# Kernel tuning notes

Hardware: AMD Instinct MI355X
Metric: run time of the kernel (lower is better)

Reference implementation:

```python
import jax, jax.numpy as jnp
import numpy as np

H = 1024  # lstm_hidden_dim
E = 1024  # embedding_size
T = 512   # seq_len
B = 128   # batch


def setup_inputs() -> dict:
    key = jax.random.key(0)
    k0, k1, k2, k3 = jax.random.split(key, 4)
    bound = 1.0 / np.sqrt(H)
    embeds = jax.random.normal(k0, (T, B, E), dtype=jnp.float32)
    # Stacked gate weights in order [g, i, f, o]; same math as 8 separate GEMMs.
    W_x = jax.random.uniform(k1, (E, 4 * H), jnp.float32, -bound, bound)
    W_h = jax.random.uniform(k2, (H, 4 * H), jnp.float32, -bound, bound)
    b = jax.random.uniform(k3, (4 * H,), jnp.float32, -bound, bound)
    b = b.at[2 * H:3 * H].add(1.0)  # forget-gate bias +1
    return {"embeds": embeds, "W_x": W_x, "W_h": W_h, "b": b}


def reference(embeds, W_x, W_h, b):
    Tn, Bn, _ = embeds.shape
    # Batch all input projections into one big GEMM (same math as per-step GEMMs).
    xproj = jnp.einsum('tbe,ef->tbf', embeds, W_x) + b  # [T, B, 4H]
    h0 = jnp.zeros((Bn, H), embeds.dtype)
    c0 = jnp.zeros((Bn, H), embeds.dtype)

    def step(carry, xp):
        h, c = carry
        z = xp + h @ W_h  # [B, 4H]
        g = jnp.tanh(z[:, :H])
        i = jax.nn.sigmoid(z[:, H:2 * H])
        f = jax.nn.sigmoid(z[:, 2 * H:3 * H])
        o = jax.nn.sigmoid(z[:, 3 * H:])
        c_new = g * i + c * f
        h_new = jnp.tanh(c_new) * o
        # Original module records h BEFORE the update at step t (h_prev).
        return (h_new, c_new), h

    _, h_total = jax.lax.scan(step, (h0, c0), xproj)
    return h_total  # [T, B, H], h_total[0] is zeros
```

## Files before the change

kernel.cpp:

```cpp
#include <hip/hip_runtime.h>
#include <hip/hip_bf16.h>

typedef __attribute__((ext_vector_type(8)))  short          bf16x8;
typedef __attribute__((ext_vector_type(4)))  float          f32x4;
typedef __attribute__((ext_vector_type(8)))  unsigned short us8;

__device__ __forceinline__ unsigned short f2b(float f) {
  union { __hip_bfloat16 h; unsigned short u; } v;
  v.h = __float2bfloat16(f);
  return v.u;
}
__device__ __forceinline__ float b2f(unsigned short u) {
  union { unsigned u; float f; } v; v.u = ((unsigned)u) << 16; return v.f;
}
__device__ __forceinline__ float sigf(float x) {
  return __builtin_amdgcn_rcpf(1.f + __expf(-x));
}
__device__ __forceinline__ float tanhf_(float x) {
  return 2.f * __builtin_amdgcn_rcpf(1.f + __expf(-2.f * x)) - 1.f;
}


__global__ __launch_bounds__(256) void conv_e(const float* __restrict__ in,
                                              unsigned short* __restrict__ out) {
  const size_t i = ((size_t)blockIdx.x * 256 + threadIdx.x) * 8;
  const float4 v0 = *(const float4*)(in + i);
  const float4 v1 = *(const float4*)(in + i + 4);
  us8 o;
  o[0]=f2b(v0.x); o[1]=f2b(v0.y); o[2]=f2b(v0.z); o[3]=f2b(v0.w);
  o[4]=f2b(v1.x); o[5]=f2b(v1.y); o[6]=f2b(v1.z); o[7]=f2b(v1.w);
  *(us8*)(out + i) = o;
}

__global__ __launch_bounds__(256) void conv_wT(const float* __restrict__ W,
                                               unsigned short* __restrict__ WT) {
  __shared__ float tile[64][65];
  const int bx = blockIdx.x & 63;
  const int by = blockIdx.x >> 6;
  const int tc = threadIdx.x & 63, tr = threadIdx.x >> 6;
  #pragma unroll
  for (int i = 0; i < 16; ++i) {
    const int r = i * 4 + tr;
    tile[r][tc] = W[(size_t)(by * 64 + r) * 4096 + bx * 64 + tc];
  }
  __syncthreads();
  #pragma unroll
  for (int i = 0; i < 16; ++i) {
    const int c = i * 4 + tr;
    WT[(size_t)(bx * 64 + c) * 1024 + by * 64 + tc] = f2b(tile[tc][c]);
  }
}

__global__ __launch_bounds__(256) void conv_whp(const float* __restrict__ Wh,
                                                unsigned short* __restrict__ Wp) {
  const int id = blockIdx.x * 256 + threadIdx.x;
  const int l  = id & 63;
  const int kt = (id >> 6) & 7;
  const int nt = (id >> 9) & 7;
  const int kq = (id >> 12) & 3;
  const int n  = id >> 14;
  const int zi = nt * 16 + (l & 15);
  const int col = (zi >> 5) * 1024 + n * 32 + (zi & 31);
  const int k0 = kq * 256 + kt * 32 + (l >> 4) * 8;
  us8 o;
  #pragma unroll
  for (int j = 0; j < 8; ++j) o[j] = f2b(Wh[(size_t)(k0 + j) * 4096 + col]);
  *(us8*)(Wp + (size_t)id * 8) = o;
}

__global__ __launch_bounds__(256) void gemm_xproj(const unsigned short* __restrict__ A,
                                                  const unsigned short* __restrict__ B,
                                                  const float* __restrict__ bias,
                                                  unsigned short* __restrict__ C) {
  __shared__ unsigned short Alds[128 * 64];
  __shared__ unsigned short Blds[128 * 64];
  const int tid = threadIdx.x, lane = tid & 63, wv = tid >> 6;
  const int wm = wv >> 1, wn = wv & 1;
  const int sid = (blockIdx.x & 7) * 2048 + (blockIdx.x >> 3);
  const int bn = sid & 31, bm = sid >> 5;
  f32x4 acc[4][4] = {};
  const int srow = wv * 8 + (lane >> 3);
  const int sinner = (lane & 7) * 8;
  for (int kt = 0; kt < 16; ++kt) {
    #pragma unroll
    for (int rd = 0; rd < 4; ++rd) {
      const int row = rd * 32 + srow;
      const unsigned short* ga = A + (size_t)(bm * 128 + row) * 1024 + kt * 64 + sinner;
      const unsigned short* gb = B + (size_t)(bn * 128 + row) * 1024 + kt * 64 + sinner;
      __builtin_amdgcn_global_load_lds(
          (const __attribute__((address_space(1))) unsigned short*)ga,
          (__attribute__((address_space(3))) unsigned short*)(Alds + rd * 2048 + wv * 512),
          16, 0, 0);
      __builtin_amdgcn_global_load_lds(
          (const __attribute__((address_space(1))) unsigned short*)gb,
          (__attribute__((address_space(3))) unsigned short*)(Blds + rd * 2048 + wv * 512),
          16, 0, 0);
    }
    __syncthreads();
    #pragma unroll
    for (int ks = 0; ks < 2; ++ks) {
      const int kk = ks * 32 + (lane >> 4) * 8;
      bf16x8 af[4], bfr[4];
      #pragma unroll
      for (int mt = 0; mt < 4; ++mt)
        af[mt] = *(const bf16x8*)(Alds + (wm * 64 + mt * 16 + (lane & 15)) * 64 + kk);
      #pragma unroll
      for (int nt = 0; nt < 4; ++nt)
        bfr[nt] = *(const bf16x8*)(Blds + (wn * 64 + nt * 16 + (lane & 15)) * 64 + kk);
      #pragma unroll
      for (int mt = 0; mt < 4; ++mt)
        #pragma unroll
        for (int nt = 0; nt < 4; ++nt)
          acc[mt][nt] = __builtin_amdgcn_mfma_f32_16x16x32_bf16(af[mt], bfr[nt], acc[mt][nt], 0, 0, 0);
    }
    __syncthreads();
  }
  #pragma unroll
  for (int mt = 0; mt < 4; ++mt) {
    const int row0 = bm * 128 + wm * 64 + mt * 16 + (lane >> 4) * 4;
    #pragma unroll
    for (int nt = 0; nt < 4; ++nt) {
      const int col = bn * 128 + wn * 64 + nt * 16 + (lane & 15);
      const float bv = bias[col];
      #pragma unroll
      for (int r = 0; r < 4; ++r)
        C[(size_t)(row0 + r) * 4096 + col] = f2b(acc[mt][nt][r] + bv);
    }
  }
}

__global__ __launch_bounds__(256, 1) void lstm_recur(
    const unsigned short* __restrict__ xproj,
    const unsigned short* __restrict__ Wp,
    unsigned short* __restrict__ hbuf,
    float* __restrict__ out,
    unsigned* __restrict__ flags) {
  __shared__ float zpart[10][16][132];
  const int tid = threadIdx.x;
  const int lane = tid & 63;
  const int kq = tid >> 6;
  const int m = blockIdx.x >> 5;
  const int n = blockIdx.x & 31;

  bf16x8 wf[64];
  {
    const unsigned short* wb = Wp + ((size_t)(n * 4 + kq) * 64) * 512 + lane * 8;
    #pragma unroll
    for (int f = 0; f < 64; ++f) wf[f] = *(const bf16x8*)(wb + f * 512);
  }

  const int r    = tid >> 4;
  const int hg   = tid & 15;
  const int hc0  = n * 32 + hg * 2;
  const int grow = m * 16 + r;

  float cr0 = 0.f, cr1 = 0.f;
  const size_t xbase = (size_t)grow * 4096 + hc0;
  unsigned* bcast = flags + (m * 32 + (lane & 31)) * 32 + n;
  const unsigned* myf = flags + (size_t)(m * 32 + n) * 32 + kq * 8 + (lane & 7);

  unsigned xu0, xu1, xu2, xu3;
  {
    const unsigned short* xpp = xproj + xbase;
    asm volatile("global_load_dword %0, %1, off" : "=v"(xu0) : "v"(xpp));
    asm volatile("global_load_dword %0, %1, off" : "=v"(xu1) : "v"(xpp + 1024));
    asm volatile("global_load_dword %0, %1, off" : "=v"(xu2) : "v"(xpp + 2048));
    asm volatile("global_load_dword %0, %1, off" : "=v"(xu3) : "v"(xpp + 3072));
  }

  const size_t aoff = ((size_t)(m * 16 + (lane & 15))) * 1024 + kq * 256 + (lane >> 4) * 8;

  for (int t = 0; t < 511; ++t) {
    const unsigned short* ab = hbuf + (t & 1) * 131072 + aoff;

    bf16x8 av0, av1, av2, av3, av4, av5, av6, av7;
    __builtin_amdgcn_sched_barrier(0);
    asm volatile("global_load_dwordx4 %0, %1, off sc0 sc1"            : "=v"(av0) : "v"(ab));
    asm volatile("global_load_dwordx4 %0, %1, off offset:64 sc0 sc1"  : "=v"(av1) : "v"(ab));
    asm volatile("global_load_dwordx4 %0, %1, off offset:128 sc0 sc1" : "=v"(av2) : "v"(ab));
    asm volatile("global_load_dwordx4 %0, %1, off offset:192 sc0 sc1" : "=v"(av3) : "v"(ab));
    asm volatile("global_load_dwordx4 %0, %1, off offset:256 sc0 sc1" : "=v"(av4) : "v"(ab));
    asm volatile("global_load_dwordx4 %0, %1, off offset:320 sc0 sc1" : "=v"(av5) : "v"(ab));
    asm volatile("global_load_dwordx4 %0, %1, off offset:384 sc0 sc1" : "=v"(av6) : "v"(ab));
    asm volatile("global_load_dwordx4 %0, %1, off offset:448 sc0 sc1" : "=v"(av7) : "v"(ab));
    asm volatile("s_waitcnt vmcnt(0)" ::: "memory");
    __builtin_amdgcn_sched_barrier(0);

    f32x4 ac0 = {0.f,0.f,0.f,0.f}, ac1 = {0.f,0.f,0.f,0.f};
    f32x4 ac2 = {0.f,0.f,0.f,0.f}, ac3 = {0.f,0.f,0.f,0.f};
    f32x4 ac4 = {0.f,0.f,0.f,0.f}, ac5 = {0.f,0.f,0.f,0.f};
    f32x4 ac6 = {0.f,0.f,0.f,0.f}, ac7 = {0.f,0.f,0.f,0.f};
#define MF_STEP(AV, KT) \
    ac0 = __builtin_amdgcn_mfma_f32_16x16x32_bf16(AV, wf[ 0 + KT], ac0, 0, 0, 0); \
    ac1 = __builtin_amdgcn_mfma_f32_16x16x32_bf16(AV, wf[ 8 + KT], ac1, 0, 0, 0); \
    ac2 = __builtin_amdgcn_mfma_f32_16x16x32_bf16(AV, wf[16 + KT], ac2, 0, 0, 0); \
    ac3 = __builtin_amdgcn_mfma_f32_16x16x32_bf16(AV, wf[24 + KT], ac3, 0, 0, 0); \
    ac4 = __builtin_amdgcn_mfma_f32_16x16x32_bf16(AV, wf[32 + KT], ac4, 0, 0, 0); \
    ac5 = __builtin_amdgcn_mfma_f32_16x16x32_bf16(AV, wf[40 + KT], ac5, 0, 0, 0); \
    ac6 = __builtin_amdgcn_mfma_f32_16x16x32_bf16(AV, wf[48 + KT], ac6, 0, 0, 0); \
    ac7 = __builtin_amdgcn_mfma_f32_16x16x32_bf16(AV, wf[56 + KT], ac7, 0, 0, 0);
    MF_STEP(av0, 0) MF_STEP(av1, 1) MF_STEP(av2, 2) MF_STEP(av3, 3)
    MF_STEP(av4, 4) MF_STEP(av5, 5) MF_STEP(av6, 6) MF_STEP(av7, 7)
#undef MF_STEP

    {
      const int crow = (lane >> 4) * 4, ccol = lane & 15;
#define DUMP(NT, AC) \
      zpart[kq][crow + 0][NT * 16 + ccol] = AC[0]; \
      zpart[kq][crow + 1][NT * 16 + ccol] = AC[1]; \
      zpart[kq][crow + 2][NT * 16 + ccol] = AC[2]; \
      zpart[kq][crow + 3][NT * 16 + ccol] = AC[3];
      DUMP(0, ac0) DUMP(1, ac1) DUMP(2, ac2) DUMP(3, ac3)
      DUMP(4, ac4) DUMP(5, ac5) DUMP(6, ac6) DUMP(7, ac7)
#undef DUMP
    }
    __syncthreads();

    float zc[4][2];
    #pragma unroll
    for (int g = 0; g < 4; ++g)
      #pragma unroll
      for (int j = 0; j < 2; ++j) {
        const int col = g * 32 + hg * 2 + j;
        zc[g][j] = (zpart[0][r][col] + zpart[1][r][col])
                 + (zpart[2][r][col] + zpart[3][r][col]);
      }

    float hv0, hv1;
    {
      const float zg = zc[0][0] + b2f((unsigned short)(xu0 & 0xffffu));
      const float zi = zc[1][0] + b2f((unsigned short)(xu1 & 0xffffu));
      const float zf = zc[2][0] + b2f((unsigned short)(xu2 & 0xffffu));
      const float zo = zc[3][0] + b2f((unsigned short)(xu3 & 0xffffu));
      cr0 = tanhf_(zg) * sigf(zi) + cr0 * sigf(zf);
      hv0 = tanhf_(cr0) * sigf(zo);
    }
    {
      const float zg = zc[0][1] + b2f((unsigned short)(xu0 >> 16));
      const float zi = zc[1][1] + b2f((unsigned short)(xu1 >> 16));
      const float zf = zc[2][1] + b2f((unsigned short)(xu2 >> 16));
      const float zo = zc[3][1] + b2f((unsigned short)(xu3 >> 16));
      cr1 = tanhf_(zg) * sigf(zi) + cr1 * sigf(zf);
      hv1 = tanhf_(cr1) * sigf(zo);
    }

    if (t < 510) {
      const unsigned hp = (unsigned)f2b(hv0) | ((unsigned)f2b(hv1) << 16);
      unsigned short* hd = hbuf + ((t & 1) ^ 1) * 131072 + (size_t)grow * 1024 + hc0;
      asm volatile("global_store_dword %0, %1, off sc0 sc1" :: "v"(hd), "v"(hp) : "memory");
      asm volatile("s_waitcnt vmcnt(0)" ::: "memory");
      __syncthreads();
      if (kq == 0 && lane < 32) {
        const unsigned g1 = (unsigned)(t + 1);
        asm volatile("global_store_dword %0, %1, off sc0 sc1" :: "v"(bcast), "v"(g1) : "memory");
      }
    }

    float2 ho; ho.x = hv0; ho.y = hv1;
    *(float2*)(out + ((size_t)(t + 1) * 128 + grow) * 1024 + hc0) = ho;

    if (t < 510) {
      const unsigned short* xpp = xproj + (size_t)(t + 1) * 524288 + xbase;
      asm volatile("global_load_dword %0, %1, off" : "=v"(xu0) : "v"(xpp));
      asm volatile("global_load_dword %0, %1, off" : "=v"(xu1) : "v"(xpp + 1024));
      asm volatile("global_load_dword %0, %1, off" : "=v"(xu2) : "v"(xpp + 2048));
      asm volatile("global_load_dword %0, %1, off" : "=v"(xu3) : "v"(xpp + 3072));
      unsigned v;
      do {
        asm volatile("global_load_dword %0, %1, off sc0 sc1" : "=v"(v) : "v"(myf));
        asm volatile("s_waitcnt vmcnt(0)" ::: "memory");
      } while (__any((int)v <= t));
    }
  }
}

extern "C" void kernel_launch(void* const* d_in, const int* in_sizes, int n_in,
                              void* d_out, int out_size, void* d_ws, size_t ws_size,
                              hipStream_t stream) {
  (void)in_sizes; (void)n_in; (void)out_size; (void)ws_size;
  const float* embeds = (const float*)d_in[0];
  const float* Wx     = (const float*)d_in[1];
  const float* Wh     = (const float*)d_in[2];
  const float* bias   = (const float*)d_in[3];
  float* out = (float*)d_out;

  char* w = (char*)d_ws;
  unsigned short* eb  = (unsigned short*)(w);
  unsigned short* WxT = (unsigned short*)(w + 134217728);
  unsigned short* Whp = (unsigned short*)(w + 142606336);
  unsigned short* xp  = (unsigned short*)(w + 150994944);
  unsigned short* hb  = (unsigned short*)(w + 687865856);
  unsigned*       fl  = (unsigned*)(w + 688390144);

  hipMemsetAsync(d_out, 0, (size_t)128 * 1024 * sizeof(float), stream);
  hipMemsetAsync(hb, 0, 524288, stream);
  hipMemsetAsync(fl, 0, 32768, stream);

  conv_e    <<<32768, 256, 0, stream>>>(embeds, eb);
  conv_wT   <<<1024,  256, 0, stream>>>(Wx, WxT);
  conv_whp  <<<2048,  256, 0, stream>>>(Wh, Whp);
  gemm_xproj<<<16384, 256, 0, stream>>>(eb, WxT, bias, xp);
  lstm_recur<<<256,   256, 0, stream>>>(xp, Whp, hb, out, fl);
}
```

Baseline: 2.919 ms.

## Pre-swizzle GEMM operands into MFMA fragment layout and drop LDS staging

The three conversion kernels are merged into one launch. It writes embeds and W_x in bf16 already packed in the per-lane MFMA fragment order. The xproj GEMM is replaced by an LDS-free kernel in which each wave loads its fragments straight from global memory as contiguous 16-byte vectors and computes a 64x128 tile. This removes the LDS staging and the barriers, at the cost of more global and L2 traffic because blocks share no operand reuse.

```diff
diff --git a/kernel.cpp b/kernel.cpp
--- a/kernel.cpp
+++ b/kernel.cpp
@@ -20,111 +20,98 @@
   return 2.f * __builtin_amdgcn_rcpf(1.f + __expf(-2.f * x)) - 1.f;
 }
 
-
-__global__ __launch_bounds__(256) void conv_e(const float* __restrict__ in,
-                                              unsigned short* __restrict__ out) {
-  const size_t i = ((size_t)blockIdx.x * 256 + threadIdx.x) * 8;
-  const float4 v0 = *(const float4*)(in + i);
-  const float4 v1 = *(const float4*)(in + i + 4);
-  us8 o;
-  o[0]=f2b(v0.x); o[1]=f2b(v0.y); o[2]=f2b(v0.z); o[3]=f2b(v0.w);
-  o[4]=f2b(v1.x); o[5]=f2b(v1.y); o[6]=f2b(v1.z); o[7]=f2b(v1.w);
-  *(us8*)(out + i) = o;
-}
-
-__global__ __launch_bounds__(256) void conv_wT(const float* __restrict__ W,
-                                               unsigned short* __restrict__ WT) {
-  __shared__ float tile[64][65];
-  const int bx = blockIdx.x & 63;
-  const int by = blockIdx.x >> 6;
-  const int tc = threadIdx.x & 63, tr = threadIdx.x >> 6;
+__global__ __launch_bounds__(256) void conv_all(const float* __restrict__ embeds,
+                                                const float* __restrict__ Wx,
+                                                const float* __restrict__ Wh,
+                                                unsigned short* __restrict__ ebf,
+                                                unsigned short* __restrict__ wxf,
+                                                unsigned short* __restrict__ whp) {
+  const int b = blockIdx.x;
+  if (b < 32768) {
+    const int id = b * 256 + threadIdx.x;
+    const int l  = id & 63;
+    const int kt = (id >> 6) & 31;
+    const int rt = id >> 11;
+    const size_t src = ((size_t)(rt * 16 + (l & 15))) * 1024 + kt * 32 + (l >> 4) * 8;
+    const float4 v0 = *(const float4*)(embeds + src);
+    const float4 v1 = *(const float4*)(embeds + src + 4);
+    us8 o;
+    o[0]=f2b(v0.x); o[1]=f2b(v0.y); o[2]=f2b(v0.z); o[3]=f2b(v0.w);
+    o[4]=f2b(v1.x); o[5]=f2b(v1.y); o[6]=f2b(v1.z); o[7]=f2b(v1.w);
+    *(us8*)(ebf + (size_t)id * 8) = o;
+  } else if (b < 34816) {
+    const int id = (b - 32768) * 256 + threadIdx.x;
+    const int l  = id & 63;
+    const int kt = (id >> 6) & 31;
+    const int c  = id >> 11;
+    const int col = c * 16 + (l & 15);
+    const int k0 = kt * 32 + (l >> 4) * 8;
+    us8 o;
+    #pragma unroll
+    for (int j = 0; j < 8; ++j) o[j] = f2b(Wx[(size_t)(k0 + j) * 4096 + col]);
+    *(us8*)(wxf + (size_t)id * 8) = o;
+  } else {
+    const int id = (b - 34816) * 256 + threadIdx.x;
+    const int l  = id & 63;
+    const int kt = (id >> 6) & 7;
+    const int nt = (id >> 9) & 7;
+    const int kq = (id >> 12) & 3;
+    const int n  = id >> 14;
+    const int zi = nt * 16 + (l & 15);
+    const int col = (zi >> 5) * 1024 + n * 32 + (zi & 31);
+    const int k0 = kq * 256 + kt * 32 + (l >> 4) * 8;
+    us8 o;
+    #pragma unroll
+    for (int j = 0; j < 8; ++j) o[j] = f2b(Wh[(size_t)(k0 + j) * 4096 + col]);
+    *(us8*)(whp + (size_t)id * 8) = o;
+  }
+}
+
+__global__ __launch_bounds__(256, 2) void gemm_xproj_reg(
+    const unsigned short* __restrict__ ebf,
+    const unsigned short* __restrict__ wxf,
+    const float* __restrict__ bias,
+    unsigned short* __restrict__ xp) {
+  const int lane = threadIdx.x & 63;
+  const int wv = threadIdx.x >> 6;
+  const int w = blockIdx.x * 4 + wv;
+  const int ct = w & 31;
+  const int rt = w >> 5;
+
+  float bvf[8];
   #pragma unroll
-  for (int i = 0; i < 16; ++i) {
-    const int r = i * 4 + tr;
-    tile[r][tc] = W[(size_t)(by * 64 + r) * 4096 + bx * 64 + tc];
-  }
-  __syncthreads();
+  for (int nt = 0; nt < 8; ++nt) bvf[nt] = bias[ct * 128 + nt * 16 + (lane & 15)];
+
+  f32x4 acc[4][8];
   #pragma unroll
-  for (int i = 0; i < 16; ++i) {
-    const int c = i * 4 + tr;
-    WT[(size_t)(bx * 64 + c) * 1024 + by * 64 + tc] = f2b(tile[tc][c]);
-  }
-}
-
-__global__ __launch_bounds__(256) void conv_whp(const float* __restrict__ Wh,
-                                                unsigned short* __restrict__ Wp) {
-  const int id = blockIdx.x * 256 + threadIdx.x;
-  const int l  = id & 63;
-  const int kt = (id >> 6) & 7;
-  const int nt = (id >> 9) & 7;
-  const int kq = (id >> 12) & 3;
-  const int n  = id >> 14;
-  const int zi = nt * 16 + (l & 15);
-  const int col = (zi >> 5) * 1024 + n * 32 + (zi & 31);
-  const int k0 = kq * 256 + kt * 32 + (l >> 4) * 8;
-  us8 o;
+  for (int a = 0; a < 4; ++a)
+    #pragma unroll
+    for (int nt = 0; nt < 8; ++nt) acc[a][nt] = f32x4{0.f,0.f,0.f,0.f};
+
+  for (int kt = 0; kt < 32; ++kt) {
+    bf16x8 af[4], bfr[8];
+    #pragma unroll
+    for (int a = 0; a < 4; ++a)
+      af[a] = *(const bf16x8*)(ebf + (size_t)((4 * rt + a) * 32 + kt) * 512 + lane * 8);
+    #pragma unroll
+    for (int nt = 0; nt < 8; ++nt)
+      bfr[nt] = *(const bf16x8*)(wxf + (size_t)((ct * 8 + nt) * 32 + kt) * 512 + lane * 8);
+    #pragma unroll
+    for (int a = 0; a < 4; ++a)
+      #pragma unroll
+      for (int nt = 0; nt < 8; ++nt)
+        acc[a][nt] = __builtin_amdgcn_mfma_f32_16x16x32_bf16(af[a], bfr[nt], acc[a][nt], 0, 0, 0);
+  }
+
   #pragma unroll
-  for (int j = 0; j < 8; ++j) o[j] = f2b(Wh[(size_t)(k0 + j) * 4096 + col]);
-  *(us8*)(Wp + (size_t)id * 8) = o;
-}
-
-__global__ __launch_bounds__(256) void gemm_xproj(const unsigned short* __restrict__ A,
-                                                  const unsigned short* __restrict__ B,
-                                                  const float* __restrict__ bias,
-                                                  unsigned short* __restrict__ C) {
-  __shared__ unsigned short Alds[128 * 64];
-  __shared__ unsigned short Blds[128 * 64];
-  const int tid = threadIdx.x, lane = tid & 63, wv = tid >> 6;
-  const int wm = wv >> 1, wn = wv & 1;
-  const int sid = (blockIdx.x & 7) * 2048 + (blockIdx.x >> 3);
-  const int bn = sid & 31, bm = sid >> 5;
-  f32x4 acc[4][4] = {};
-  const int srow = wv * 8 + (lane >> 3);
-  const int sinner = (lane & 7) * 8;
-  for (int kt = 0; kt < 16; ++kt) {
-    #pragma unroll
-    for (int rd = 0; rd < 4; ++rd) {
-      const int row = rd * 32 + srow;
-      const unsigned short* ga = A + (size_t)(bm * 128 + row) * 1024 + kt * 64 + sinner;
-      const unsigned short* gb = B + (size_t)(bn * 128 + row) * 1024 + kt * 64 + sinner;
-      __builtin_amdgcn_global_load_lds(
-          (const __attribute__((address_space(1))) unsigned short*)ga,
-          (__attribute__((address_space(3))) unsigned short*)(Alds + rd * 2048 + wv * 512),
-          16, 0, 0);
-      __builtin_amdgcn_global_load_lds(
-          (const __attribute__((address_space(1))) unsigned short*)gb,
-          (__attribute__((address_space(3))) unsigned short*)(Blds + rd * 2048 + wv * 512),
-          16, 0, 0);
-    }
-    __syncthreads();
-    #pragma unroll
-    for (int ks = 0; ks < 2; ++ks) {
-      const int kk = ks * 32 + (lane >> 4) * 8;
-      bf16x8 af[4], bfr[4];
+  for (int a = 0; a < 4; ++a) {
+    const int row0 = rt * 64 + a * 16 + (lane >> 4) * 4;
+    #pragma unroll
+    for (int nt = 0; nt < 8; ++nt) {
+      const int col = ct * 128 + nt * 16 + (lane & 15);
       #pragma unroll
-      for (int mt = 0; mt < 4; ++mt)
-        af[mt] = *(const bf16x8*)(Alds + (wm * 64 + mt * 16 + (lane & 15)) * 64 + kk);
-      #pragma unroll
-      for (int nt = 0; nt < 4; ++nt)
-        bfr[nt] = *(const bf16x8*)(Blds + (wn * 64 + nt * 16 + (lane & 15)) * 64 + kk);
-      #pragma unroll
-      for (int mt = 0; mt < 4; ++mt)
-        #pragma unroll
-        for (int nt = 0; nt < 4; ++nt)
-          acc[mt][nt] = __builtin_amdgcn_mfma_f32_16x16x32_bf16(af[mt], bfr[nt], acc[mt][nt], 0, 0, 0);
-    }
-    __syncthreads();
-  }
-  #pragma unroll
-  for (int mt = 0; mt < 4; ++mt) {
-    const int row0 = bm * 128 + wm * 64 + mt * 16 + (lane >> 4) * 4;
-    #pragma unroll
-    for (int nt = 0; nt < 4; ++nt) {
-      const int col = bn * 128 + wn * 64 + nt * 16 + (lane & 15);
-      const float bv = bias[col];
-      #pragma unroll
-      for (int r = 0; r < 4; ++r)
-        C[(size_t)(row0 + r) * 4096 + col] = f2b(acc[mt][nt][r] + bv);
+      for (int rr = 0; rr < 4; ++rr)
+        xp[(size_t)(row0 + rr) * 4096 + col] = f2b(acc[a][nt][rr] + bvf[nt]);
     }
   }
 }
@@ -285,10 +272,10 @@
   float* out = (float*)d_out;
 
   char* w = (char*)d_ws;
-  unsigned short* eb  = (unsigned short*)(w);
-  unsigned short* WxT = (unsigned short*)(w + 134217728);
-  unsigned short* Whp = (unsigned short*)(w + 142606336);
-  unsigned short* xp  = (unsigned short*)(w + 150994944);
+  unsigned short* ebf = (unsigned short*)(w);
+  unsigned short* wxf = (unsigned short*)(w + 134217728);
+  unsigned short* whp = (unsigned short*)(w + 142606336);
+  unsigned short* xpb = (unsigned short*)(w + 150994944);
   unsigned short* hb  = (unsigned short*)(w + 687865856);
   unsigned*       fl  = (unsigned*)(w + 688390144);
 
@@ -296,9 +283,7 @@
   hipMemsetAsync(hb, 0, 524288, stream);
   hipMemsetAsync(fl, 0, 32768, stream);
 
-  conv_e    <<<32768, 256, 0, stream>>>(embeds, eb);
-  conv_wT   <<<1024,  256, 0, stream>>>(Wx, WxT);
-  conv_whp  <<<2048,  256, 0, stream>>>(Wh, Whp);
-  gemm_xproj<<<16384, 256, 0, stream>>>(eb, WxT, bias, xp);
-  lstm_recur<<<256,   256, 0, stream>>>(xp, Whp, hb, out, fl);
-}
+  conv_all      <<<36864, 256, 0, stream>>>(embeds, Wx, Wh, ebf, wxf, whp);
+  gemm_xproj_reg<<<8192,  256, 0, stream>>>(ebf, wxf, bias, xpb);
+  lstm_recur    <<<256,   256, 0, stream>>>(xpb, whp, hb, out, fl);
+}
```

Result: faster. 2.829 ms (-3.1%).
